# Optimization experiments

Hardware: AMD Instinct MI355X
Metric: run time of the kernel (lower is better)

## Reference

```python
import jax, jax.numpy as jnp
import numpy as np

B, N, F, H, K, C = 2048, 62, 512, 128, 2, 2
EPS_BN = 1e-5
EPS_NORM = 1e-10
N_TRIL = N * (N + 1) // 2  # 1953, tril_indices incl. diagonal
FC_SIZES = [H * N, H * N // 2, H * N // 4, H * N // 8, C]  # [7936,3968,1984,992,2]


def setup_inputs() -> dict:
    key = jax.random.key(0)
    ks = jax.random.split(key, 16)
    inp = {
        "x": jax.random.normal(ks[0], (B, N, F), jnp.float32),
        "edge_weight": jax.random.uniform(ks[1], (N_TRIL,), jnp.float32),
        "bn_gamma": jnp.ones((F,), jnp.float32),
        "bn_beta": jnp.zeros((F,), jnp.float32),
        # xavier_normal for SGConv lin
        "lin_w": jax.random.normal(ks[2], (H, F), jnp.float32) * (2.0 / (F + H)) ** 0.5,
        "lin_b": jnp.zeros((H,), jnp.float32),
    }
    for i in range(4):
        fan_in, fan_out = FC_SIZES[i], FC_SIZES[i + 1]
        inp[f"fc{i}_w"] = jax.random.normal(ks[3 + i], (fan_out, fan_in), jnp.float32) * (2.0 / (fan_in + fan_out)) ** 0.5
        inp[f"fc{i}_b"] = jnp.zeros((fan_out,), jnp.float32)
    return inp


def _normalized_adj(edge_weight):
    """Build symmetric dense adjacency from tril params, normalize_matrix
    (relu + sym deg-norm), then SGConv.norm (D^-1/2 A D^-1/2; self-loops are
    already on the diagonal so add_remaining_self_loops is a no-op)."""
    xs, ys = np.tril_indices(N)
    Wm = jnp.zeros((N, N), jnp.float32).at[xs, ys].set(edge_weight)
    Wm = Wm + Wm.T - jnp.diag(jnp.diag(Wm))
    A = jax.nn.relu(Wm)
    dinv = jax.lax.rsqrt(A.sum(1) + EPS_NORM)
    A = dinv[:, None] * A * dinv[None, :]
    # SGConv normalization: deg = scatter_add over rows -> row sums
    deg = A.sum(1)
    dis = jnp.where(deg > 0, deg ** -0.5, 0.0)
    return dis[:, None] * A * dis[None, :]


def reference(x, edge_weight, bn_gamma, bn_beta, lin_w, lin_b,
              fc0_w, fc0_b, fc1_w, fc1_b, fc2_w, fc2_b, fc3_w, fc3_b):
    A = _normalized_adj(edge_weight)  # [N, N], shared across batch
    # BatchNorm1d over feature channels, stats over (batch, node) dims (train mode)
    mean = x.mean((0, 1))
    var = x.var((0, 1))
    h = (x - mean) * jax.lax.rsqrt(var + EPS_BN) * bn_gamma + bn_beta  # [B,N,F]
    # K-hop SGConv propagation == dense matmul with shared normalized adjacency
    for _ in range(K):
        h = jnp.einsum('ij,bjf->bif', A, h)
    h = h @ lin_w.T + lin_b           # [B, N, H]
    h = h.reshape(B, N * H)           # node-major flatten, matches x.view(batch,-1)
    # dropout is identity in eval mode
    for W, b in ((fc0_w, fc0_b), (fc1_w, fc1_b), (fc2_w, fc2_b)):
        h = jax.nn.relu(h @ W.T + b)
    return h @ fc3_w.T + fc3_b        # [B, C]
```

## Files before the change

kernel.cpp:

```cpp
#include <hip/hip_runtime.h>

typedef _Float16 f16;
typedef __attribute__((ext_vector_type(4))) _Float16 f16x4;
typedef __attribute__((ext_vector_type(8))) _Float16 f16x8;
typedef __attribute__((ext_vector_type(4))) float f32x4;

#define DEVI static __device__ __forceinline__

DEVI void async_copy16(const f16* g, f16* l) {
  __builtin_amdgcn_global_load_lds(
      (const __attribute__((address_space(1))) void*)g,
      (__attribute__((address_space(3))) void*)l, 16, 0, 0);
}

#define MEMPIN asm volatile("" ::: "memory")
#define RBAR __builtin_amdgcn_s_barrier()

__global__ __launch_bounds__(1024) void k_adj(const float* __restrict__ ew, float* __restrict__ out)
{
  __shared__ float sW[62][64];
  __shared__ float sT[62][64];
  __shared__ float d[62];
  const int tid = threadIdx.x;
  for (int idx = tid; idx < 62 * 62; idx += 1024) {
    int i = idx / 62, j = idx % 62;
    float w = (j <= i) ? ew[i * (i + 1) / 2 + j] : ew[j * (j + 1) / 2 + i];
    sW[i][j] = fmaxf(w, 0.f);
  }
  __syncthreads();
  if (tid < 62) {
    float s = 0.f;
    for (int j = 0; j < 62; j++) s += sW[tid][j];
    d[tid] = rsqrtf(s + 1e-10f);
  }
  __syncthreads();
  for (int idx = tid; idx < 62 * 62; idx += 1024) {
    int i = idx / 62, j = idx % 62;
    sW[i][j] *= d[i] * d[j];
  }
  __syncthreads();
  if (tid < 62) {
    float s = 0.f;
    for (int j = 0; j < 62; j++) s += sW[tid][j];
    d[tid] = (s > 0.f) ? rsqrtf(s) : 0.f;
  }
  __syncthreads();
  for (int idx = tid; idx < 62 * 62; idx += 1024) {
    int i = idx / 62, j = idx % 62;
    sW[i][j] *= d[i] * d[j];
  }
  __syncthreads();
  for (int idx = tid; idx < 62 * 64; idx += 1024) {
    int i = idx >> 6, j = idx & 63;
    float s = 0.f;
    if (j < 62) {
      for (int k = 0; k < 62; k++) s += sW[i][k] * sW[k][j];
    }
    sT[i][j] = s;
    out[idx] = s;
  }
  __syncthreads();
  if (tid < 62) {
    float s = 0.f;
    for (int j = 0; j < 62; j++) s += sT[tid][j];
    out[62 * 64 + tid] = s;
  }
}

__global__ __launch_bounds__(1024) void k_bnstats(const float* __restrict__ X, float* __restrict__ part)
{
  const int tid = threadIdx.x;
  const int c4 = (tid & 127) << 2;
  const int rg = tid >> 7;
  float sx = 0, sy = 0, sz = 0, sw = 0, qx = 0, qy = 0, qz = 0, qw = 0;
  const long r0 = (long)blockIdx.x * 496 + rg;
  for (int i = 0; i < 62; i++) {
    const float4 v = *(const float4*)(X + (r0 + 8 * i) * 512 + c4);
    sx += v.x; sy += v.y; sz += v.z; sw += v.w;
    qx += v.x * v.x; qy += v.y * v.y; qz += v.z * v.z; qw += v.w * v.w;
  }
  __shared__ float red[1024][8];
  red[tid][0] = sx; red[tid][1] = sy; red[tid][2] = sz; red[tid][3] = sw;
  red[tid][4] = qx; red[tid][5] = qy; red[tid][6] = qz; red[tid][7] = qw;
  __syncthreads();
  if (tid < 128) {
    float acc8[8];
#pragma unroll
    for (int j = 0; j < 8; j++) acc8[j] = 0.f;
#pragma unroll
    for (int g = 0; g < 8; g++)
#pragma unroll
      for (int j = 0; j < 8; j++) acc8[j] += red[g * 128 + tid][j];
    float* p = part + (long)blockIdx.x * 1024;
#pragma unroll
    for (int j = 0; j < 4; j++) p[c4 + j] = acc8[j];
#pragma unroll
    for (int j = 0; j < 4; j++) p[512 + c4 + j] = acc8[4 + j];
  }
}

__global__ __launch_bounds__(512) void k_bnfin(const float* __restrict__ part, const float* __restrict__ g,
                                               const float* __restrict__ be, float* __restrict__ ssb)
{
  const int c = threadIdx.x;
  float s = 0.f, q = 0.f;
  for (int b = 0; b < 256; b++) {
    s += part[b * 1024 + c];
    q += part[b * 1024 + 512 + c];
  }
  const float inv = 1.f / 126976.f;
  const float mean = s * inv;
  const float var = q * inv - mean * mean;
  const float sc = g[c] * rsqrtf(var + 1e-5f);
  ssb[c] = sc;
  ssb[512 + c] = be[c] - mean * sc;
}

__global__ __launch_bounds__(256) void k_foldw1(const float* __restrict__ lw, const float* __restrict__ ssb,
                                                f16* __restrict__ w1h, float* __restrict__ b1p)
{
  const int h = blockIdx.x;
  const int tid = threadIdx.x;
  float partl = 0.f;
  for (int f = tid; f < 512; f += 256) {
    const float w = lw[h * 512 + f];
    w1h[h * 512 + f] = (f16)(w * ssb[f]);
    partl += w * ssb[512 + f];
  }
  __shared__ float red[256];
  red[tid] = partl;
  __syncthreads();
  for (int s = 128; s; s >>= 1) {
    if (tid < s) red[tid] += red[tid + s];
    __syncthreads();
  }
  if (tid == 0) b1p[h] = red[0];
}

__global__ __launch_bounds__(256) void k_cvtw(const float* __restrict__ src, f16* __restrict__ dst,
                                              int N, int K, int Npad, int Kpad)
{
  const long total4 = (long)Npad * Kpad / 4;
  const int kp4 = Kpad >> 2;
  for (long i = (long)blockIdx.x * 256 + threadIdx.x; i < total4; i += (long)gridDim.x * 256) {
    const long n = i / kp4;
    const int k = (int)(i % kp4) << 2;
    f16x4 h;
    if (n < N && k < K) {
      const float4 v = *(const float4*)(src + n * K + k);
      h[0] = (f16)v.x; h[1] = (f16)v.y; h[2] = (f16)v.z; h[3] = (f16)v.w;
    } else {
      h[0] = (f16)0.f; h[1] = (f16)0.f; h[2] = (f16)0.f; h[3] = (f16)0.f;
    }
    *(f16x4*)(dst + i * 4) = h;
  }
}

__global__ __launch_bounds__(256, 2) void k_linprop(
    const float* __restrict__ X, const f16* __restrict__ Bw,
    const float* __restrict__ A2, const float* __restrict__ b1p,
    const float* __restrict__ lb, f16* __restrict__ Z)
{
  __shared__ f16 smem[128 * 128];
  __shared__ float sA2[62 * 64];
  __shared__ float sR[62];
  __shared__ float sB1[128];
  __shared__ float sLB[128];
  f16* sA = smem;
  f16* sB = smem + 8192;
  const int tid = threadIdx.x;
  const int lane = tid & 63;
  const int wave = tid >> 6;
  const int wr = wave >> 1, wc = wave & 1;
  const long rowA0 = (long)blockIdx.x * 124;

  for (int i = tid; i < 992; i += 256)
    *(float4*)&sA2[i * 4] = *(const float4*)(A2 + i * 4);
  if (tid < 62) sR[tid] = A2[3968 + tid];
  if (tid < 128) sB1[tid] = b1p[tid];
  if (tid >= 128) sLB[tid - 128] = lb[tid - 128];

  const int srow = tid >> 3;
  const int scolb = (tid & 7) << 4;
  const int gcolb = scolb ^ ((srow & 7) << 4);
  const f16* gB = Bw + (long)srow * 512 + (gcolb >> 1);
  f16* lB = sB + srow * 64 + (scolb >> 1);

  const int ac4 = tid & 15;
  const int ar0 = tid >> 4;
  const int aswz = (ar0 & 7) << 4;
  char* lAbase = (char*)sA + ar0 * 128 + ((ac4 * 8) ^ aswz);

  const int frow = lane & 15;
  const int kb = (lane >> 4) << 4;
  const int rswz = (lane & 7) << 4;

  f32x4 acc[4][4] = {};

  for (int kt = 0; kt < 512; kt += 64) {
#pragma unroll
    for (int i = 0; i < 8; i++) {
      long rr = rowA0 + ar0 + 16 * i;
      if (rr > 126975) rr = 126975;
      const float4 v = *(const float4*)(X + rr * 512 + kt + ac4 * 4);
      f16x4 hh;
      hh[0] = (f16)v.x; hh[1] = (f16)v.y; hh[2] = (f16)v.z; hh[3] = (f16)v.w;
      *(f16x4*)(lAbase + 16 * i * 128) = hh;
    }
#pragma unroll
    for (int i = 0; i < 4; i++)
      async_copy16(gB + kt + (long)i * (32 * 512), lB + i * 2048);
    __syncthreads();
#pragma unroll
    for (int kk = 0; kk < 2; kk++) {
      f16x8 af[4], bf[4];
#pragma unroll
      for (int m = 0; m < 4; m++) {
        const int row = wr * 64 + m * 16 + frow;
        af[m] = *(const f16x8*)((const char*)sA + row * 128 + ((kk * 64 + kb) ^ rswz));
      }
#pragma unroll
      for (int n = 0; n < 4; n++) {
        const int row = wc * 64 + n * 16 + frow;
        bf[n] = *(const f16x8*)((const char*)sB + row * 128 + ((kk * 64 + kb) ^ rswz));
      }
#pragma unroll
      for (int m = 0; m < 4; m++)
#pragma unroll
        for (int n = 0; n < 4; n++)
          acc[m][n] = __builtin_amdgcn_mfma_f32_16x16x32_f16(af[m], bf[n], acc[m][n], 0, 0, 0);
    }
    __syncthreads();
  }

  const int crow = wr * 64 + ((lane >> 4) << 2);
  const int ccol = wc * 64 + (lane & 15);
#pragma unroll
  for (int n = 0; n < 4; n++)
#pragma unroll
    for (int m = 0; m < 4; m++)
#pragma unroll
      for (int r = 0; r < 4; r++)
        smem[(crow + m * 16 + r) * 128 + ccol + n * 16] = (f16)acc[m][n][r];
  __syncthreads();

  const int h = tid & 127;
  const int g = tid >> 7;
  float yc[62];
#pragma unroll
  for (int j = 0; j < 62; j++) yc[j] = (float)smem[(g * 62 + j) * 128 + h];
  const float bh1 = sB1[h];
  const float bh2 = sLB[h];
  f16* zp = Z + ((long)blockIdx.x * 2 + g) * 7936 + h;
  for (int n = 0; n < 62; n++) {
    float s = 0.f;
#pragma unroll
    for (int j = 0; j < 62; j++) s += sA2[n * 64 + j] * yc[j];
    zp[n * 128] = (f16)(s + sR[n] * bh1 + bh2);
  }
}

template <int LOOPN, int MT, int NT, int KS>
__global__ __launch_bounds__(512, 2) void k_fc8(
    const f16* __restrict__ A, const f16* __restrict__ Bw, f16* __restrict__ P,
    const int K, const int kslice, const int PLD)
{
  __shared__ f16 sA[2][256 * 64];
  __shared__ f16 sB[2][256 * 64];
  const int tid = threadIdx.x;
  const int bid = blockIdx.x;
  const int xcd = bid & 7, ii = bid >> 3;
  int nt, mt, ks;
  if constexpr (NT == 16) {
    nt = xcd * 2 + (ii & 1); mt = (ii >> 1) & (MT - 1); ks = ii >> 4;
  } else {
    nt = xcd; mt = ii & (MT - 1); ks = ii >> 3;
  }
  const long rowA0 = (long)mt * 256;
  const long rowB0 = (long)nt * 256;
  const long k0 = (long)ks * kslice;

  const int srow = tid >> 3;
  const int scolb = (tid & 7) << 4;
  const int gcolb = scolb ^ ((srow & 7) << 4);
  const f16* gA = A + (rowA0 + srow) * (long)K + k0 + (gcolb >> 1);
  const f16* gB = Bw + (rowB0 + srow) * (long)K + k0 + (gcolb >> 1);

#define SGA(d, q, kt) async_copy16(gA + (kt) + (long)(q) * 64 * K, &sA[d][0] + (q) * 4096 + tid * 8)
#define SGB(d, q, kt) async_copy16(gB + (kt) + (long)(q) * 64 * K, &sB[d][0] + (q) * 4096 + tid * 8)

  const int lane = tid & 63;
  const int wave = tid >> 6;
  const int wr = wave >> 2;
  const int wc = wave & 3;
  const int frow = lane & 15;
  const int kb = (lane >> 4) << 4;
  const int rsw = (frow & 7) << 4;

  f32x4 acc[8][4] = {};
  f16x8 af[4][2], bf[4][2];

#define RDA(d, mh) do { _Pragma("unroll") for (int m_ = 0; m_ < 4; m_++) {                      \
    const int row_ = wr * 128 + (mh) * 64 + m_ * 16 + frow;                                     \
    af[m_][0] = *(const f16x8*)((const char*)&sA[d][0] + row_ * 128 + (kb ^ rsw));              \
    af[m_][1] = *(const f16x8*)((const char*)&sA[d][0] + row_ * 128 + ((64 + kb) ^ rsw)); } } while (0)
#define RDB(d) do { _Pragma("unroll") for (int n_ = 0; n_ < 4; n_++) {                          \
    const int row_ = wc * 64 + n_ * 16 + frow;                                                  \
    bf[n_][0] = *(const f16x8*)((const char*)&sB[d][0] + row_ * 128 + (kb ^ rsw));              \
    bf[n_][1] = *(const f16x8*)((const char*)&sB[d][0] + row_ * 128 + ((64 + kb) ^ rsw)); } } while (0)
#define QUAD(mh, nh) do { _Pragma("unroll") for (int m_ = 0; m_ < 4; m_++)                      \
    _Pragma("unroll") for (int n_ = 0; n_ < 2; n_++) {                                          \
      acc[(mh)*4+m_][(nh)*2+n_] = __builtin_amdgcn_mfma_f32_16x16x32_f16(af[m_][0], bf[(nh)*2+n_][0], acc[(mh)*4+m_][(nh)*2+n_], 0, 0, 0); \
      acc[(mh)*4+m_][(nh)*2+n_] = __builtin_amdgcn_mfma_f32_16x16x32_f16(af[m_][1], bf[(nh)*2+n_][1], acc[(mh)*4+m_][(nh)*2+n_], 0, 0, 0); } } while (0)
#define VMW8 asm volatile("s_waitcnt vmcnt(8)" ::: "memory")
#define VMW0 asm volatile("s_waitcnt vmcnt(0)" ::: "memory")
#define PRIO1 __builtin_amdgcn_s_setprio(1)
#define PRIO0 __builtin_amdgcn_s_setprio(0)

  SGA(0, 0, 0); SGA(0, 2, 0); SGB(0, 0, 0); SGB(0, 1, 0);
  SGA(0, 1, 0); SGA(0, 3, 0); SGB(0, 2, 0); SGB(0, 3, 0);
  SGA(1, 0, 64); SGA(1, 2, 64); SGB(1, 0, 64); SGB(1, 1, 64);
  SGA(1, 1, 64); SGA(1, 3, 64); SGB(1, 2, 64); SGB(1, 3, 64);

  for (int t = 0; t < LOOPN; ++t) {
    const long kt2 = (long)(t + 1) * 128;
    VMW8; MEMPIN; RBAR; MEMPIN;
    RDA(0, 0); RDB(0);
    PRIO1; QUAD(0, 0); PRIO0;
    MEMPIN; RBAR; MEMPIN;
    SGA(0, 0, kt2); SGA(0, 2, kt2); SGB(0, 0, kt2); SGB(0, 1, kt2);
    QUAD(0, 1);
    RDA(0, 1);
    QUAD(1, 0);
    MEMPIN; RBAR; MEMPIN;
    SGA(0, 1, kt2); SGA(0, 3, kt2); SGB(0, 2, kt2); SGB(0, 3, kt2);
    QUAD(1, 1);
    VMW8; MEMPIN; RBAR; MEMPIN;
    RDA(1, 0); RDB(1);
    PRIO1; QUAD(0, 0); PRIO0;
    MEMPIN; RBAR; MEMPIN;
    SGA(1, 0, kt2 + 64); SGA(1, 2, kt2 + 64); SGB(1, 0, kt2 + 64); SGB(1, 1, kt2 + 64);
    QUAD(0, 1);
    RDA(1, 1);
    QUAD(1, 0);
    MEMPIN; RBAR; MEMPIN;
    SGA(1, 1, kt2 + 64); SGA(1, 3, kt2 + 64); SGB(1, 2, kt2 + 64); SGB(1, 3, kt2 + 64);
    QUAD(1, 1);
  }
  VMW8; MEMPIN; RBAR; MEMPIN;
  RDA(0, 0); RDB(0);
  PRIO1; QUAD(0, 0); QUAD(0, 1); PRIO0;
  RDA(0, 1);
  PRIO1; QUAD(1, 0); QUAD(1, 1); PRIO0;
  VMW0; MEMPIN; RBAR; MEMPIN;
  RDA(1, 0); RDB(1);
  PRIO1; QUAD(0, 0); QUAD(0, 1); PRIO0;
  RDA(1, 1);
  PRIO1; QUAD(1, 0); QUAD(1, 1); PRIO0;

  f16* Pp = P + (long)ks * 2048 * PLD;
#pragma unroll
  for (int mi = 0; mi < 8; mi++) {
    const long r0 = rowA0 + wr * 128 + (mi >> 2) * 64 + (mi & 3) * 16 + ((lane >> 4) << 2);
#pragma unroll
    for (int n = 0; n < 4; n++) {
      const long col = rowB0 + wc * 64 + n * 16 + (lane & 15);
#pragma unroll
      for (int r = 0; r < 4; r++)
        Pp[(r0 + r) * PLD + col] = (f16)acc[mi][n][r];
    }
  }
#undef SGA
#undef SGB
#undef RDA
#undef RDB
#undef QUAD
#undef VMW8
#undef VMW0
#undef PRIO1
#undef PRIO0
}

template <int S>
__global__ __launch_bounds__(256) void k_fixs(const f16* __restrict__ P, const float* __restrict__ b,
                                              f16* __restrict__ C, int N, int realN)
{
  const long total = 2048L * N;
  const int mask = N - 1;
  const long stride = (long)gridDim.x * 256 * 8;
  for (long i = ((long)blockIdx.x * 256 + threadIdx.x) * 8; i < total; i += stride) {
    float s[8];
#pragma unroll
    for (int j = 0; j < 8; j++) s[j] = 0.f;
#pragma unroll
    for (int ps = 0; ps < S; ps++) {
      const f16x8 p = *(const f16x8*)(P + (long)ps * total + i);
#pragma unroll
      for (int j = 0; j < 8; j++) s[j] += (float)p[j];
    }
    const int col = (int)(i & mask);
    f16x8 o;
#pragma unroll
    for (int j = 0; j < 8; j++) {
      const int c = col + j;
      const float bb = (c < realN) ? b[c] : 0.f;
      o[j] = (f16)fmaxf(s[j] + bb, 0.f);
    }
    *(f16x8*)(C + i) = o;
  }
}

template <int RELU, int KS>
__global__ __launch_bounds__(256, 2) void k_gemm_f16(
    const f16* __restrict__ A, const f16* __restrict__ B,
    const float* __restrict__ bias, f16* __restrict__ C,
    int N, int K, int realN)
{
  __shared__ f16 sA[128 * 64];
  __shared__ f16 sB[128 * 64];
  const int tid = threadIdx.x;
  const int lane = tid & 63;
  const int wave = tid >> 6;
  const int wr = wave >> 1, wc = wave & 1;
  const int bid = blockIdx.x;
  const int xcd = bid & 7, idx = bid >> 3;
  const long rowA0 = (long)(xcd * 2 + (idx & 1)) * 128;
  long rowB0;
  int ks;
  if constexpr (KS == 2) {
    rowB0 = (long)((idx >> 1) & 7) * 128;
    ks = idx >> 4;
  } else {
    rowB0 = (long)(idx >> 1) * 128;
    ks = 0;
  }
  const int kslice = K / KS;
  const long k0 = (long)ks * kslice;

  const int srow = tid >> 3;
  const int scolb = (tid & 7) << 4;
  const int gcolb = scolb ^ ((srow & 7) << 4);
  const f16* gA = A + (rowA0 + srow) * (long)K + k0 + (gcolb >> 1);
  const f16* gB = B + (rowB0 + srow) * (long)K + k0 + (gcolb >> 1);
  f16* lA = sA + srow * 64 + (scolb >> 1);
  f16* lB = sB + srow * 64 + (scolb >> 1);
  const long rstep = 32L * K;

  const int frow = lane & 15;
  const int kb = (lane >> 4) << 4;
  const int rswz = (lane & 7) << 4;

  f32x4 acc[4][4] = {};

  for (int kt = 0; kt < kslice; kt += 64) {
#pragma unroll
    for (int i = 0; i < 4; i++) {
      async_copy16(gA + kt + i * rstep, lA + i * 2048);
      async_copy16(gB + kt + i * rstep, lB + i * 2048);
    }
    __syncthreads();
#pragma unroll
    for (int kk = 0; kk < 2; kk++) {
      f16x8 af[4], bf[4];
#pragma unroll
      for (int m = 0; m < 4; m++) {
        const int row = wr * 64 + m * 16 + frow;
        af[m] = *(const f16x8*)((const char*)sA + row * 128 + ((kk * 64 + kb) ^ rswz));
      }
#pragma unroll
      for (int n = 0; n < 4; n++) {
        const int row = wc * 64 + n * 16 + frow;
        bf[n] = *(const f16x8*)((const char*)sB + row * 128 + ((kk * 64 + kb) ^ rswz));
      }
#pragma unroll
      for (int m = 0; m < 4; m++)
#pragma unroll
        for (int n = 0; n < 4; n++)
          acc[m][n] = __builtin_amdgcn_mfma_f32_16x16x32_f16(af[m], bf[n], acc[m][n], 0, 0, 0);
    }
    __syncthreads();
  }

  const int crow = wr * 64 + ((lane >> 4) << 2);
  const int ccol = wc * 64 + (lane & 15);
  if constexpr (KS == 1) {
#pragma unroll
    for (int n = 0; n < 4; n++) {
      const int col = (int)rowB0 + ccol + n * 16;
      const float bb = (col < realN) ? bias[col] : 0.f;
#pragma unroll
      for (int m = 0; m < 4; m++) {
        const long gr = rowA0 + crow + m * 16;
#pragma unroll
        for (int r = 0; r < 4; r++) {
          float v = acc[m][n][r] + bb;
          if (RELU) v = fmaxf(v, 0.f);
          C[(gr + r) * N + col] = (f16)v;
        }
      }
    }
  } else {
    f16* Pp = C + (long)ks * 2048 * N;
#pragma unroll
    for (int n = 0; n < 4; n++) {
      const long col = rowB0 + ccol + n * 16;
#pragma unroll
      for (int m = 0; m < 4; m++) {
        const long gr = rowA0 + crow + m * 16;
#pragma unroll
        for (int r = 0; r < 4; r++)
          Pp[(gr + r) * N + col] = (f16)acc[m][n][r];
      }
    }
  }
}

__global__ __launch_bounds__(256) void k_fc3(const f16* __restrict__ H, const float* __restrict__ W,
                                             const float* __restrict__ b, float* __restrict__ out)
{
  const int row = blockIdx.x * 4 + (threadIdx.x >> 6);
  const int lane = threadIdx.x & 63;
  const f16* h = H + (long)row * 1024;
  float a0 = 0.f, a1 = 0.f;
  for (int k = lane; k < 992; k += 64) {
    const float v = (float)h[k];
    a0 += v * W[k];
    a1 += v * W[992 + k];
  }
  for (int off = 32; off; off >>= 1) {
    a0 += __shfl_down(a0, off);
    a1 += __shfl_down(a1, off);
  }
  if (lane == 0) {
    out[row * 2 + 0] = a0 + b[0];
    out[row * 2 + 1] = a1 + b[1];
  }
}

extern "C" void kernel_launch(void* const* d_in, const int* in_sizes, int n_in,
                              void* d_out, int out_size, void* d_ws, size_t ws_size,
                              hipStream_t stream)
{
  const float* x    = (const float*)d_in[0];
  const float* ew   = (const float*)d_in[1];
  const float* bng  = (const float*)d_in[2];
  const float* bnb  = (const float*)d_in[3];
  const float* linw = (const float*)d_in[4];
  const float* linb = (const float*)d_in[5];
  const float* w0   = (const float*)d_in[6];
  const float* b0   = (const float*)d_in[7];
  const float* w1   = (const float*)d_in[8];
  const float* b1   = (const float*)d_in[9];
  const float* w2   = (const float*)d_in[10];
  const float* b2   = (const float*)d_in[11];
  const float* w3   = (const float*)d_in[12];
  const float* b3   = (const float*)d_in[13];
  float* out = (float*)d_out;
  char* ws = (char*)d_ws;

  constexpr size_t oA2  = 0;
  constexpr size_t oSS  = 16384;
  constexpr size_t oB1P = 20480;
  constexpr size_t oW1H = 20992;
  constexpr size_t oP   = 152064;
  constexpr size_t oACC = oP;
  constexpr size_t oZ   = 33706496;
  constexpr size_t oW0H = 66212352;
  constexpr size_t WS_NEED = 131224064;
  constexpr size_t oH0  = oZ;
  constexpr size_t oW1F = oZ + 16777216;
  constexpr size_t oH1  = 67260928;
  constexpr size_t oW2F = 75649536;
  constexpr size_t oH2  = 79843840;
  if (ws_size < WS_NEED) return;

  float* A2  = (float*)(ws + oA2);
  float* acc = (float*)(ws + oACC);
  float* ssb = (float*)(ws + oSS);
  float* b1p = (float*)(ws + oB1P);
  f16* w1h = (f16*)(ws + oW1H);
  f16* P   = (f16*)(ws + oP);
  f16* Z   = (f16*)(ws + oZ);
  f16* w0h = (f16*)(ws + oW0H);
  f16* h0  = (f16*)(ws + oH0);
  f16* w1f = (f16*)(ws + oW1F);
  f16* h1  = (f16*)(ws + oH1);
  f16* w2f = (f16*)(ws + oW2F);
  f16* h2  = (f16*)(ws + oH2);

  k_adj<<<1, 1024, 0, stream>>>(ew, A2);
  k_bnstats<<<256, 1024, 0, stream>>>(x, acc);
  k_bnfin<<<1, 512, 0, stream>>>(acc, bng, bnb, ssb);
  k_foldw1<<<128, 256, 0, stream>>>(linw, ssb, w1h, b1p);
  k_cvtw<<<1024, 256, 0, stream>>>(w0, w0h, 3968, 7936, 4096, 7936);
  k_linprop<<<1024, 256, 0, stream>>>(x, w1h, A2, b1p, linb, Z);
  k_fc8<30, 8, 16, 2><<<256, 512, 0, stream>>>(Z, w0h, P, 7936, 3968, 4096);
  k_fixs<2><<<2048, 256, 0, stream>>>(P, b0, h0, 4096, 3968);
  k_cvtw<<<512, 256, 0, stream>>>(w1, w1f, 1984, 3968, 2048, 4096);
  k_cvtw<<<256, 256, 0, stream>>>(w2, w2f, 992, 1984, 1024, 2048);
  k_fc8<7, 8, 8, 4><<<256, 512, 0, stream>>>(h0, w1f, P, 4096, 1024, 2048);
  k_fixs<4><<<1024, 256, 0, stream>>>(P, b1, h1, 2048, 1984);
  k_gemm_f16<1, 2><<<256, 256, 0, stream>>>(h1, w2f, b2, P, 1024, 2048, 992);
  k_fixs<2><<<512, 256, 0, stream>>>(P, b2, h2, 1024, 992);
  k_fc3<<<512, 256, 0, stream>>>(h2, w3, b3, out);
}
```

Baseline: 465.1 us.

## Switch fc8 GEMM to 32x32x16 MFMA, merge weight conversions, raise linprop occupancy

The main fc GEMM kernel's inner loop now uses 32x32x16 MFMA tiles with 16-wide accumulators instead of 16x16x32. This cuts the number of LDS fragment reads and MFMA issues per tile, and the epilogue store mapping is changed to match. Separately, the two fc1/fc2 weight-conversion launches are merged into a single kernel to save one launch. The linprop kernel's launch bounds are raised to 3 blocks per CU, which limits its registers and risks spills.

```diff
diff --git a/kernel.cpp b/kernel.cpp
--- a/kernel.cpp
+++ b/kernel.cpp
@@ -4,6 +4,7 @@
 typedef __attribute__((ext_vector_type(4))) _Float16 f16x4;
 typedef __attribute__((ext_vector_type(8))) _Float16 f16x8;
 typedef __attribute__((ext_vector_type(4))) float f32x4;
+typedef __attribute__((ext_vector_type(16))) float f32x16;
 
 #define DEVI static __device__ __forceinline__
 
@@ -137,12 +138,12 @@
   if (tid == 0) b1p[h] = red[0];
 }
 
-__global__ __launch_bounds__(256) void k_cvtw(const float* __restrict__ src, f16* __restrict__ dst,
-                                              int N, int K, int Npad, int Kpad)
+DEVI void cvt_body(const float* __restrict__ src, f16* __restrict__ dst,
+                   int N, int K, int Npad, int Kpad, int bix, int nblk)
 {
   const long total4 = (long)Npad * Kpad / 4;
   const int kp4 = Kpad >> 2;
-  for (long i = (long)blockIdx.x * 256 + threadIdx.x; i < total4; i += (long)gridDim.x * 256) {
+  for (long i = (long)bix * 256 + threadIdx.x; i < total4; i += (long)nblk * 256) {
     const long n = i / kp4;
     const int k = (int)(i % kp4) << 2;
     f16x4 h;
@@ -156,7 +157,20 @@
   }
 }
 
-__global__ __launch_bounds__(256, 2) void k_linprop(
+__global__ __launch_bounds__(256) void k_cvtw(const float* __restrict__ src, f16* __restrict__ dst,
+                                              int N, int K, int Npad, int Kpad)
+{
+  cvt_body(src, dst, N, K, Npad, Kpad, blockIdx.x, gridDim.x);
+}
+
+__global__ __launch_bounds__(256) void k_cvtw2(const float* __restrict__ s1, f16* __restrict__ d1,
+                                               const float* __restrict__ s2, f16* __restrict__ d2)
+{
+  if (blockIdx.x < 512) cvt_body(s1, d1, 1984, 3968, 2048, 4096, blockIdx.x, 512);
+  else                  cvt_body(s2, d2, 992, 1984, 1024, 2048, blockIdx.x - 512, 256);
+}
+
+__global__ __launch_bounds__(256, 3) void k_linprop(
     const float* __restrict__ X, const f16* __restrict__ Bw,
     const float* __restrict__ A2, const float* __restrict__ b1p,
     const float* __restrict__ lb, f16* __restrict__ Z)
@@ -293,25 +307,24 @@
   const int wave = tid >> 6;
   const int wr = wave >> 2;
   const int wc = wave & 3;
-  const int frow = lane & 15;
-  const int kb = (lane >> 4) << 4;
-  const int rsw = (frow & 7) << 4;
-
-  f32x4 acc[8][4] = {};
-  f16x8 af[4][2], bf[4][2];
-
-#define RDA(d, mh) do { _Pragma("unroll") for (int m_ = 0; m_ < 4; m_++) {                      \
-    const int row_ = wr * 128 + (mh) * 64 + m_ * 16 + frow;                                     \
-    af[m_][0] = *(const f16x8*)((const char*)&sA[d][0] + row_ * 128 + (kb ^ rsw));              \
-    af[m_][1] = *(const f16x8*)((const char*)&sA[d][0] + row_ * 128 + ((64 + kb) ^ rsw)); } } while (0)
-#define RDB(d) do { _Pragma("unroll") for (int n_ = 0; n_ < 4; n_++) {                          \
-    const int row_ = wc * 64 + n_ * 16 + frow;                                                  \
-    bf[n_][0] = *(const f16x8*)((const char*)&sB[d][0] + row_ * 128 + (kb ^ rsw));              \
-    bf[n_][1] = *(const f16x8*)((const char*)&sB[d][0] + row_ * 128 + ((64 + kb) ^ rsw)); } } while (0)
-#define QUAD(mh, nh) do { _Pragma("unroll") for (int m_ = 0; m_ < 4; m_++)                      \
-    _Pragma("unroll") for (int n_ = 0; n_ < 2; n_++) {                                          \
-      acc[(mh)*4+m_][(nh)*2+n_] = __builtin_amdgcn_mfma_f32_16x16x32_f16(af[m_][0], bf[(nh)*2+n_][0], acc[(mh)*4+m_][(nh)*2+n_], 0, 0, 0); \
-      acc[(mh)*4+m_][(nh)*2+n_] = __builtin_amdgcn_mfma_f32_16x16x32_f16(af[m_][1], bf[(nh)*2+n_][1], acc[(mh)*4+m_][(nh)*2+n_], 0, 0, 0); } } while (0)
+  const int r31 = lane & 31;
+  const int hi16 = (lane >> 5) << 4;
+  const int rsw = (lane & 7) << 4;
+
+  f32x16 acc[4][2] = {};
+  f16x8 af[2][4], bf[2][4];
+
+#define RDA(d, mh) do { _Pragma("unroll") for (int m_ = 0; m_ < 2; m_++) {                      \
+    const int row_ = wr * 128 + (mh) * 64 + m_ * 32 + r31;                                      \
+    _Pragma("unroll") for (int ks_ = 0; ks_ < 4; ks_++)                                         \
+      af[m_][ks_] = *(const f16x8*)((const char*)&sA[d][0] + row_ * 128 + ((ks_ * 32 + hi16) ^ rsw)); } } while (0)
+#define RDB(d) do { _Pragma("unroll") for (int n_ = 0; n_ < 2; n_++) {                          \
+    const int row_ = wc * 64 + n_ * 32 + r31;                                                   \
+    _Pragma("unroll") for (int ks_ = 0; ks_ < 4; ks_++)                                         \
+      bf[n_][ks_] = *(const f16x8*)((const char*)&sB[d][0] + row_ * 128 + ((ks_ * 32 + hi16) ^ rsw)); } } while (0)
+#define QUAD(mh, nh) do { _Pragma("unroll") for (int ks_ = 0; ks_ < 4; ks_++)                   \
+    _Pragma("unroll") for (int m_ = 0; m_ < 2; m_++)                                            \
+      acc[(mh)*2+m_][nh] = __builtin_amdgcn_mfma_f32_32x32x16_f16(af[m_][ks_], bf[nh][ks_], acc[(mh)*2+m_][nh], 0, 0, 0); } while (0)
 #define VMW8 asm volatile("s_waitcnt vmcnt(8)" ::: "memory")
 #define VMW0 asm volatile("s_waitcnt vmcnt(0)" ::: "memory")
 #define PRIO1 __builtin_amdgcn_s_setprio(1)
@@ -360,14 +373,16 @@
 
   f16* Pp = P + (long)ks * 2048 * PLD;
 #pragma unroll
-  for (int mi = 0; mi < 8; mi++) {
-    const long r0 = rowA0 + wr * 128 + (mi >> 2) * 64 + (mi & 3) * 16 + ((lane >> 4) << 2);
-#pragma unroll
-    for (int n = 0; n < 4; n++) {
-      const long col = rowB0 + wc * 64 + n * 16 + (lane & 15);
-#pragma unroll
-      for (int r = 0; r < 4; r++)
-        Pp[(r0 + r) * PLD + col] = (f16)acc[mi][n][r];
+  for (int mi = 0; mi < 4; mi++) {
+    const long rbase = rowA0 + wr * 128 + mi * 32 + 4 * (lane >> 5);
+#pragma unroll
+    for (int nh = 0; nh < 2; nh++) {
+      const long col = rowB0 + wc * 64 + nh * 32 + r31;
+#pragma unroll
+      for (int r = 0; r < 16; r++) {
+        const long row = rbase + (r & 3) + 8 * (r >> 2);
+        Pp[row * PLD + col] = (f16)acc[mi][nh][r];
+      }
     }
   }
 #undef SGA
@@ -596,8 +611,7 @@
   k_linprop<<<1024, 256, 0, stream>>>(x, w1h, A2, b1p, linb, Z);
   k_fc8<30, 8, 16, 2><<<256, 512, 0, stream>>>(Z, w0h, P, 7936, 3968, 4096);
   k_fixs<2><<<2048, 256, 0, stream>>>(P, b0, h0, 4096, 3968);
-  k_cvtw<<<512, 256, 0, stream>>>(w1, w1f, 1984, 3968, 2048, 4096);
-  k_cvtw<<<256, 256, 0, stream>>>(w2, w2f, 992, 1984, 1024, 2048);
+  k_cvtw2<<<768, 256, 0, stream>>>(w1, w1f, w2, w2f);
   k_fc8<7, 8, 8, 4><<<256, 512, 0, stream>>>(h0, w1f, P, 4096, 1024, 2048);
   k_fixs<4><<<1024, 256, 0, stream>>>(P, b1, h1, 2048, 1984);
   k_gemm_f16<1, 2><<<256, 256, 0, stream>>>(h1, w2f, b2, P, 1024, 2048, 992);
```

Result: no change. 472.5 us (+1.6%).
